# Kernel tuning notes

Measured on AMD Instinct MI355X. Metric: run time of the kernel, lower is better.

The kernel has to match this reference:

```python
import jax, jax.numpy as jnp
import numpy as np

N_NODES = 50000
N_EDGES = 800000
HID = 64


def fake_quant_w(w):
    # symmetric per-tensor int8 fake quantization (num_bits=8)
    s = jnp.maximum(jnp.max(jnp.abs(w)) / 127.0, 1e-8)
    q = jnp.clip(jnp.round(w / s), -127.0, 127.0) * s
    return w + jax.lax.stop_gradient(q - w)


def layer_norm(x, g, b, eps=1e-5):
    mu = jnp.mean(x, axis=-1, keepdims=True)
    var = jnp.var(x, axis=-1, keepdims=True)
    return (x - mu) * jax.lax.rsqrt(var + eps) * g + b


def pointnet_conv(x, pos, src, dst, W, n_nodes):
    # message: cat([x_j, pos_j - pos_i]) @ W_q^T, max-aggregated at i (dst)
    rel = pos[src] - pos[dst]                       # [E, 3]
    feat = jnp.concatenate([x[src], rel], axis=-1)  # [E, C+3]
    msg = feat @ fake_quant_w(W).T                  # [E, 64]
    h = jax.ops.segment_max(msg, dst, num_segments=n_nodes)
    return jnp.where(jnp.isfinite(h), h, 0.0)       # empty segments -> 0


def setup_inputs() -> dict:
    key = jax.random.key(0)
    ks = jax.random.split(key, 16)
    d = {}
    d["x"] = jax.random.normal(ks[0], (N_NODES, 1), jnp.float32)
    d["pos"] = jax.random.normal(ks[1], (N_NODES, 3), jnp.float32)
    d["edge_index"] = jax.random.randint(ks[2], (2, N_EDGES), 0, N_NODES, jnp.int32)
    sc = 0.02
    d["W0"] = jax.random.normal(ks[3], (HID, 1 + 3), jnp.float32) * sc
    d["Ws"] = jax.random.normal(ks[4], (4, HID, HID + 3), jnp.float32) * sc
    d["ln_g"] = jnp.ones((5, HID), jnp.float32)
    d["ln_b"] = jnp.zeros((5, HID), jnp.float32)
    d["mlp_w1"] = jax.random.normal(ks[5], (128, 320), jnp.float32) * sc
    d["mlp_b1"] = jnp.zeros((128,), jnp.float32)
    d["mlp_w2"] = jax.random.normal(ks[6], (128, 128), jnp.float32) * sc
    d["mlp_b2"] = jnp.zeros((128,), jnp.float32)
    d["mlp_w3"] = jax.random.normal(ks[7], (64, 128), jnp.float32) * sc
    d["mlp_b3"] = jnp.zeros((64,), jnp.float32)
    d["mlp_w4"] = jax.random.normal(ks[8], (2, 64), jnp.float32) * sc
    d["mlp_b4"] = jnp.zeros((2,), jnp.float32)
    d["scale"] = jnp.ones((2,), jnp.float32)
    return d


def reference(x, pos, edge_index, W0, Ws, ln_g, ln_b,
              mlp_w1, mlp_b1, mlp_w2, mlp_b2, mlp_w3, mlp_b3, mlp_w4, mlp_b4,
              scale):
    src, dst = edge_index[0], edge_index[1]
    n = x.shape[0]
    embeddings = []
    h = x
    for i in range(5):
        W = W0 if i == 0 else Ws[i - 1]
        h = pointnet_conv(h, pos, src, dst, W, n)
        h = layer_norm(h, ln_g[i], ln_b[i])
        h = jax.nn.relu(h)
        embeddings.append(h)
    z = jnp.concatenate(embeddings, axis=-1)  # [N, 320]
    z = layer_norm(z, jnp.ones((z.shape[-1],), z.dtype), jnp.zeros((z.shape[-1],), z.dtype))
    z = jax.nn.relu(z @ mlp_w1.T + mlp_b1)
    z = jax.nn.relu(z @ mlp_w2.T + mlp_b2)
    z = jax.nn.relu(z @ mlp_w3.T + mlp_b3)
    flow = (z @ mlp_w4.T + mlp_b4) * scale
    return flow
```

## Files before the change

kernel.cpp:

```cpp
#include <hip/hip_runtime.h>
#include <hip/hip_bf16.h>

#define N_NODES 50000
#define N_EDGES 800000
#define NBLK 196

__device__ __forceinline__ float bf2f(unsigned short u) {
    union { unsigned int i; float f; } c; c.i = ((unsigned int)u) << 16; return c.f;
}
__device__ __forceinline__ unsigned short f2bf(float f) {
    union { float f; unsigned int u; } c; c.f = f;
    unsigned int u = c.u;
    u += 0x7fffu + ((u >> 16) & 1u);
    return (unsigned short)(u >> 16);
}
__device__ __forceinline__ float ldin(const void* p, long i, int f32) {
    return f32 ? ((const float*)p)[i] : bf2f(((const unsigned short*)p)[i]);
}
__device__ __forceinline__ float wsum(float v) {
#pragma unroll
    for (int m = 32; m; m >>= 1) v += __shfl_xor(v, m, 64);
    return v;
}

__global__ void probe_kernel(const unsigned short* __restrict__ lng, int* __restrict__ flag) {
    if (threadIdx.x == 0 && blockIdx.x == 0)
        flag[0] = (lng[0] == 0x3F80 && lng[1] == 0x3F80) ? 0 : 1;
}

__global__ __launch_bounds__(256) void hist_kernel(const int* __restrict__ ei, int* __restrict__ deg) {
    int e = blockIdx.x * 256 + threadIdx.x;
    if (e < N_EDGES) atomicAdd(&deg[ei[N_EDGES + e]], 1);
}

__global__ __launch_bounds__(256) void bsum_kernel(const int* __restrict__ deg,
                                                   int* __restrict__ bsum) {
    __shared__ int wt[4];
    const int t = threadIdx.x, lane = t & 63, wid = t >> 6;
    const int i = blockIdx.x * 256 + t;
    int v = (i < N_NODES) ? deg[i] : 0;
    int r = v;
#pragma unroll
    for (int m = 32; m; m >>= 1) r += __shfl_xor(r, m, 64);
    if (lane == 0) wt[wid] = r;
    __syncthreads();
    if (t == 0) bsum[blockIdx.x] = wt[0] + wt[1] + wt[2] + wt[3];
}

__global__ __launch_bounds__(256) void boff_kernel(const int* __restrict__ bsum,
                                                   int* __restrict__ boff) {
    __shared__ int wt[4];
    const int t = threadIdx.x, lane = t & 63, wid = t >> 6;
    int v = (t < NBLK) ? bsum[t] : 0;
    int inc = v;
#pragma unroll
    for (int off = 1; off < 64; off <<= 1) {
        int u = __shfl_up(inc, off, 64);
        if (lane >= off) inc += u;
    }
    if (lane == 63) wt[wid] = inc;
    __syncthreads();
    int woff = 0;
    for (int w = 0; w < wid; ++w) woff += wt[w];
    if (t < NBLK) boff[t] = inc - v + woff;
}

__global__ __launch_bounds__(256) void scanout_kernel(const int* __restrict__ deg,
                                                      const int* __restrict__ boff,
                                                      int* __restrict__ rowptr,
                                                      int* __restrict__ cursor) {
    __shared__ int wt[4];
    const int t = threadIdx.x, lane = t & 63, wid = t >> 6;
    const int i = blockIdx.x * 256 + t;
    int v = (i < N_NODES) ? deg[i] : 0;
    int inc = v;
#pragma unroll
    for (int off = 1; off < 64; off <<= 1) {
        int u = __shfl_up(inc, off, 64);
        if (lane >= off) inc += u;
    }
    if (lane == 63) wt[wid] = inc;
    __syncthreads();
    int woff = 0;
    for (int w = 0; w < wid; ++w) woff += wt[w];
    int excl = inc - v + woff + boff[blockIdx.x];
    if (i < N_NODES) {
        rowptr[i] = excl;
        cursor[i] = excl;
        if (i == N_NODES - 1) rowptr[N_NODES] = excl + v;
    }
}

__global__ __launch_bounds__(256) void scatter_kernel(const int* __restrict__ ei,
                                                      int* __restrict__ cursor,
                                                      int* __restrict__ csr_src) {
    int e = blockIdx.x * 256 + threadIdx.x;
    if (e < N_EDGES) {
        int src = ei[e];
        int dst = ei[N_EDGES + e];
        int p = atomicAdd(&cursor[dst], 1);
        csr_src[p] = src;
    }
}

__global__ __launch_bounds__(256) void quant_kernel(const void* __restrict__ W0,
                                                    const void* __restrict__ Ws,
                                                    float* __restrict__ Wc0,
                                                    float* __restrict__ Wc,
                                                    const int* __restrict__ flagp) {
    const int f32 = *flagp;
    int layer = blockIdx.x;
    const void* src = (layer == 0) ? W0 : Ws;
    long sbase = (layer == 0) ? 0 : (long)(layer - 1) * 4288;
    float* dstc = (layer == 0) ? Wc0 : Wc + (size_t)(layer - 1) * 4352;
    int Ki = (layer == 0) ? 4 : 67;
    int n = 64 * Ki;
    __shared__ float red[256];
    float amax = 0.0f;
    for (int i = threadIdx.x; i < n; i += 256) amax = fmaxf(amax, fabsf(ldin(src, sbase + i, f32)));
    red[threadIdx.x] = amax;
    __syncthreads();
    for (int s = 128; s > 0; s >>= 1) {
        if (threadIdx.x < s) red[threadIdx.x] = fmaxf(red[threadIdx.x], red[threadIdx.x + s]);
        __syncthreads();
    }
    float sc = fmaxf(red[0] / 127.0f, 1e-8f);
    for (int i = threadIdx.x; i < n; i += 256) {
        float w = ldin(src, sbase + i, f32);
        float q = rintf(w / sc);
        q = fminf(fmaxf(q, -127.0f), 127.0f);
        int o = i / Ki, k = i % Ki;
        dstc[(size_t)k * 64 + o] = q * sc;
    }
}

__global__ __launch_bounds__(256) void u0_kernel(const void* __restrict__ x,
                                                 const void* __restrict__ pos,
                                                 const float* __restrict__ Wc0,
                                                 float* __restrict__ u,
                                                 const int* __restrict__ flagp) {
    const int f32 = *flagp;
    const int n = blockIdx.x * 256 + threadIdx.x;
    if (n >= N_NODES) return;
    const float xv = ldin(x, n, f32);
    const float p0 = ldin(pos, 3L * n + 0, f32);
    const float p1 = ldin(pos, 3L * n + 1, f32);
    const float p2 = ldin(pos, 3L * n + 2, f32);
    float4* up = reinterpret_cast<float4*>(u + (size_t)n * 64);
#pragma unroll
    for (int q = 0; q < 16; ++q) {
        const float4 w0 = *reinterpret_cast<const float4*>(Wc0 + 0 * 64 + 4 * q);
        const float4 w1 = *reinterpret_cast<const float4*>(Wc0 + 1 * 64 + 4 * q);
        const float4 w2 = *reinterpret_cast<const float4*>(Wc0 + 2 * 64 + 4 * q);
        const float4 w3 = *reinterpret_cast<const float4*>(Wc0 + 3 * 64 + 4 * q);
        float4 o;
        o.x = fmaf(p2, w3.x, fmaf(p1, w2.x, fmaf(p0, w1.x, xv * w0.x)));
        o.y = fmaf(p2, w3.y, fmaf(p1, w2.y, fmaf(p0, w1.y, xv * w0.y)));
        o.z = fmaf(p2, w3.z, fmaf(p1, w2.z, fmaf(p0, w1.z, xv * w0.z)));
        o.w = fmaf(p2, w3.w, fmaf(p1, w2.w, fmaf(p0, w1.w, xv * w0.w)));
        up[q] = o;
    }
}

__global__ __launch_bounds__(256) void agg_kernel(const float* __restrict__ u,
                                                  const void* __restrict__ pos,
                                                  const int* __restrict__ rowptr,
                                                  const int* __restrict__ csr,
                                                  const float* __restrict__ WcV, int vrow,
                                                  const float* __restrict__ WcN,
                                                  float* __restrict__ unext,
                                                  const void* __restrict__ lng,
                                                  const void* __restrict__ lnb,
                                                  int lnoff,
                                                  float* __restrict__ z, int out_off,
                                                  const int* __restrict__ flagp) {
    const int f32 = *flagp;
    const int lane = threadIdx.x & 63;
    const int n = (blockIdx.x * 256 + threadIdx.x) >> 6;
    if (n >= N_NODES) return;
    const int e0 = rowptr[n], e1 = rowptr[n + 1];
    float acc = -INFINITY;
    int e = e0;
    for (; e + 4 <= e1; e += 4) {
        const int s0 = csr[e + 0];
        const int s1 = csr[e + 1];
        const int s2 = csr[e + 2];
        const int s3 = csr[e + 3];
        const float a = u[(size_t)s0 * 64 + lane];
        const float b = u[(size_t)s1 * 64 + lane];
        const float c = u[(size_t)s2 * 64 + lane];
        const float d = u[(size_t)s3 * 64 + lane];
        acc = fmaxf(acc, fmaxf(fmaxf(a, b), fmaxf(c, d)));
    }
    for (; e < e1; ++e)
        acc = fmaxf(acc, u[(size_t)csr[e] * 64 + lane]);
    const float p0 = ldin(pos, 3L * n + 0, f32);
    const float p1 = ldin(pos, 3L * n + 1, f32);
    const float p2 = ldin(pos, 3L * n + 2, f32);
    const float v = fmaf(p2, WcV[(size_t)(vrow + 2) * 64 + lane],
                    fmaf(p1, WcV[(size_t)(vrow + 1) * 64 + lane],
                         p0 * WcV[(size_t)(vrow + 0) * 64 + lane]));
    float h = acc - v;
    if (!isfinite(h)) h = 0.0f;
    const float g = ldin(lng, lnoff + lane, f32);
    const float bb = ldin(lnb, lnoff + lane, f32);
    const float mu = wsum(h) * (1.0f / 64.0f);
    const float dd = h - mu;
    const float var = wsum(dd * dd) * (1.0f / 64.0f);
    float y = dd * rsqrtf(var + 1e-5f) * g + bb;
    y = fmaxf(y, 0.0f);
    z[(size_t)n * 320 + out_off + lane] = y;
    if (WcN) {
        float un = fmaf(p2, WcN[66 * 64 + lane],
                   fmaf(p1, WcN[65 * 64 + lane],
                        p0 * WcN[64 * 64 + lane]));
#pragma unroll
        for (int k = 0; k < 64; ++k)
            un = fmaf(__shfl(y, k, 64), WcN[k * 64 + lane], un);
        unext[(size_t)n * 64 + lane] = un;
    }
}

__global__ __launch_bounds__(256) void lnz_kernel(float* __restrict__ z) {
    const int lane = threadIdx.x & 63;
    const int gw = (blockIdx.x * blockDim.x + threadIdx.x) >> 6;
    const int nw = (gridDim.x * blockDim.x) >> 6;
    for (int nidx = gw; nidx < N_NODES; nidx += nw) {
        float v[5];
        float s = 0.f;
#pragma unroll
        for (int j = 0; j < 5; ++j) {
            v[j] = z[(size_t)nidx * 320 + j * 64 + lane];
            s += v[j];
        }
        float mu = wsum(s) * (1.0f / 320.0f);
        float q = 0.f;
#pragma unroll
        for (int j = 0; j < 5; ++j) { float d = v[j] - mu; q = fmaf(d, d, q); }
        float var = wsum(q) * (1.0f / 320.0f);
        float rs = rsqrtf(var + 1e-5f);
#pragma unroll
        for (int j = 0; j < 5; ++j) z[(size_t)nidx * 320 + j * 64 + lane] = (v[j] - mu) * rs;
    }
}

__global__ __launch_bounds__(256) void gemm_kernel(const float* __restrict__ A,
                                                   const void* __restrict__ W,
                                                   const void* __restrict__ bias,
                                                   float* __restrict__ C,
                                                   int Ki, int Ko,
                                                   const int* __restrict__ flagp) {
    __shared__ float At[16][68];
    __shared__ float Wt[16][68];
    const int f32 = *flagp;
    const int tid = threadIdx.x;
    const int bn = blockIdx.x * 64;
    const int bo = blockIdx.y * 64;
    const int o_base = (tid & 15) * 4;
    const int n_base = (tid >> 4) * 4;
    const int sr = tid >> 2;
    const int kq = (tid & 3) * 4;
    float acc[4][4] = {};
    for (int kk = 0; kk < Ki; kk += 16) {
        float4 av = make_float4(0.f, 0.f, 0.f, 0.f);
        if (bn + sr < N_NODES)
            av = *reinterpret_cast<const float4*>(A + (size_t)(bn + sr) * Ki + kk + kq);
        long wbase = (long)(bo + sr) * Ki + kk + kq;
        float wv0 = ldin(W, wbase + 0, f32);
        float wv1 = ldin(W, wbase + 1, f32);
        float wv2 = ldin(W, wbase + 2, f32);
        float wv3 = ldin(W, wbase + 3, f32);
        __syncthreads();
        At[kq + 0][sr] = av.x; At[kq + 1][sr] = av.y; At[kq + 2][sr] = av.z; At[kq + 3][sr] = av.w;
        Wt[kq + 0][sr] = wv0;  Wt[kq + 1][sr] = wv1;  Wt[kq + 2][sr] = wv2;  Wt[kq + 3][sr] = wv3;
        __syncthreads();
#pragma unroll
        for (int k = 0; k < 16; ++k) {
            const float4 a4 = *reinterpret_cast<const float4*>(&At[k][n_base]);
            const float4 w4 = *reinterpret_cast<const float4*>(&Wt[k][o_base]);
            const float a[4] = { a4.x, a4.y, a4.z, a4.w };
            const float ww[4] = { w4.x, w4.y, w4.z, w4.w };
#pragma unroll
            for (int i = 0; i < 4; ++i)
#pragma unroll
                for (int j = 0; j < 4; ++j)
                    acc[i][j] = fmaf(a[i], ww[j], acc[i][j]);
        }
    }
    float bj[4];
#pragma unroll
    for (int j = 0; j < 4; ++j) bj[j] = ldin(bias, bo + o_base + j, f32);
#pragma unroll
    for (int i = 0; i < 4; ++i) {
        int n = bn + n_base + i;
        if (n < N_NODES) {
#pragma unroll
            for (int j = 0; j < 4; ++j) {
                float c = fmaxf(acc[i][j] + bj[j], 0.0f);
                C[(size_t)n * Ko + bo + o_base + j] = c;
            }
        }
    }
}

__global__ __launch_bounds__(256) void out_kernel(const float* __restrict__ h3,
                                                  const void* __restrict__ w4,
                                                  const void* __restrict__ b4,
                                                  const void* __restrict__ scale,
                                                  void* __restrict__ out,
                                                  const int* __restrict__ flagp) {
    const int f32 = *flagp;
    const int lane = threadIdx.x & 63;
    const int gw = (blockIdx.x * blockDim.x + threadIdx.x) >> 6;
    const int nw = (gridDim.x * blockDim.x) >> 6;
    const float wa = ldin(w4, lane, f32);
    const float wb = ldin(w4, 64 + lane, f32);
    const float b0 = ldin(b4, 0, f32), b1 = ldin(b4, 1, f32);
    const float s0 = ldin(scale, 0, f32), s1 = ldin(scale, 1, f32);
    for (int nidx = gw; nidx < N_NODES; nidx += nw) {
        float h = h3[(size_t)nidx * 64 + lane];
        float d0 = wsum(h * wa);
        float d1 = wsum(h * wb);
        if (lane == 0) {
            float o0 = (d0 + b0) * s0;
            float o1 = (d1 + b1) * s1;
            if (f32) {
                ((float*)out)[nidx * 2 + 0] = o0;
                ((float*)out)[nidx * 2 + 1] = o1;
            } else {
                ((unsigned short*)out)[nidx * 2 + 0] = f2bf(o0);
                ((unsigned short*)out)[nidx * 2 + 1] = f2bf(o1);
            }
        }
    }
}

extern "C" void kernel_launch(void* const* d_in, const int* in_sizes, int n_in,
                              void* d_out, int out_size, void* d_ws, size_t ws_size,
                              hipStream_t stream) {
    (void)in_sizes; (void)n_in; (void)out_size; (void)ws_size;
    const void* x    = d_in[0];
    const void* pos  = d_in[1];
    const int*  ei   = (const int*)d_in[2];
    const void* W0   = d_in[3];
    const void* Ws   = d_in[4];
    const void* lng  = d_in[5];
    const void* lnb  = d_in[6];
    const void* w1   = d_in[7];
    const void* b1   = d_in[8];
    const void* w2   = d_in[9];
    const void* b2   = d_in[10];
    const void* w3   = d_in[11];
    const void* b3   = d_in[12];
    const void* w4   = d_in[13];
    const void* b4   = d_in[14];
    const void* scl  = d_in[15];

    float* z      = (float*)d_ws;
    float* h1     = z + 16000000;
    float* Wc0    = h1 + 6400000;
    float* Wc     = Wc0 + 256;
    int*   deg    = (int*)(Wc + 17408);
    int*   rowptr = deg + N_NODES;
    int*   cursor = rowptr + (N_NODES + 1);
    int*   flag   = cursor + N_NODES;
    int*   csr    = flag + 1;
    int*   bsum   = csr + N_EDGES;
    int*   boff   = bsum + 256;
    float* ua     = h1;
    float* ub     = h1 + 3200000;
    float* h2 = z;
    float* h3 = z + 6400000;

    hipMemsetAsync(deg, 0, N_NODES * sizeof(int), stream);
    probe_kernel<<<1, 64, 0, stream>>>((const unsigned short*)lng, flag);
    hist_kernel<<<(N_EDGES + 255) / 256, 256, 0, stream>>>(ei, deg);
    bsum_kernel<<<NBLK, 256, 0, stream>>>(deg, bsum);
    boff_kernel<<<1, 256, 0, stream>>>(bsum, boff);
    scanout_kernel<<<NBLK, 256, 0, stream>>>(deg, boff, rowptr, cursor);
    scatter_kernel<<<(N_EDGES + 255) / 256, 256, 0, stream>>>(ei, cursor, csr);
    quant_kernel<<<5, 256, 0, stream>>>(W0, Ws, Wc0, Wc, flag);

    const int gagg = (N_NODES * 64 + 255) / 256;

    u0_kernel<<<NBLK, 256, 0, stream>>>(x, pos, Wc0, ua, flag);
    agg_kernel<<<gagg, 256, 0, stream>>>(ua, pos, rowptr, csr,
                                         Wc0, 1, Wc + 0 * 4352, ub,
                                         lng, lnb, 0, z, 0, flag);
    agg_kernel<<<gagg, 256, 0, stream>>>(ub, pos, rowptr, csr,
                                         Wc + 0 * 4352, 64, Wc + 1 * 4352, ua,
                                         lng, lnb, 64, z, 64, flag);
    agg_kernel<<<gagg, 256, 0, stream>>>(ua, pos, rowptr, csr,
                                         Wc + 1 * 4352, 64, Wc + 2 * 4352, ub,
                                         lng, lnb, 128, z, 128, flag);
    agg_kernel<<<gagg, 256, 0, stream>>>(ub, pos, rowptr, csr,
                                         Wc + 2 * 4352, 64, Wc + 3 * 4352, ua,
                                         lng, lnb, 192, z, 192, flag);
    agg_kernel<<<gagg, 256, 0, stream>>>(ua, pos, rowptr, csr,
                                         Wc + 3 * 4352, 64, nullptr, nullptr,
                                         lng, lnb, 256, z, 256, flag);

    lnz_kernel<<<512, 256, 0, stream>>>(z);

    dim3 g1((N_NODES + 63) / 64, 2);
    gemm_kernel<<<g1, 256, 0, stream>>>(z, w1, b1, h1, 320, 128, flag);
    dim3 g2((N_NODES + 63) / 64, 2);
    gemm_kernel<<<g2, 256, 0, stream>>>(h1, w2, b2, h2, 128, 128, flag);
    dim3 g3((N_NODES + 63) / 64, 1);
    gemm_kernel<<<g3, 256, 0, stream>>>(h2, w3, b3, h3, 128, 64, flag);
    out_kernel<<<512, 256, 0, stream>>>(h3, w4, b4, scl, d_out, flag);
}
```

Before: 616.4 us.

## Split per-node layer transform into tiled GEMM kernel and prefetch GEMM tiles

Moves the next-layer linear transform out of the wave-per-node aggregation kernel, where it used 64 shuffles per node, into a separate LDS-tiled register-blocked GEMM kernel that reads the layer output from z, using a row-major copy of the quantized weights. It also pre-converts the MLP weights to fp32 so the GEMM kernel can use float4 loads, software-prefetches the next k-tile in the GEMM, and unrolls the gather-max loop to 8 with a scalarised node index. The cost is four extra kernel launches and an extra round trip of z and u through memory for each layer.

```diff
diff --git a/kernel.cpp b/kernel.cpp
--- a/kernel.cpp
+++ b/kernel.cpp
@@ -107,12 +107,14 @@
                                                     const void* __restrict__ Ws,
                                                     float* __restrict__ Wc0,
                                                     float* __restrict__ Wc,
+                                                    float* __restrict__ Wr,
                                                     const int* __restrict__ flagp) {
     const int f32 = *flagp;
     int layer = blockIdx.x;
     const void* src = (layer == 0) ? W0 : Ws;
     long sbase = (layer == 0) ? 0 : (long)(layer - 1) * 4288;
     float* dstc = (layer == 0) ? Wc0 : Wc + (size_t)(layer - 1) * 4352;
+    float* dstr = (layer == 0) ? nullptr : Wr + (size_t)(layer - 1) * 4352;
     int Ki = (layer == 0) ? 4 : 67;
     int n = 64 * Ki;
     __shared__ float red[256];
@@ -129,9 +131,23 @@
         float w = ldin(src, sbase + i, f32);
         float q = rintf(w / sc);
         q = fminf(fmaxf(q, -127.0f), 127.0f);
+        float v = q * sc;
         int o = i / Ki, k = i % Ki;
-        dstc[(size_t)k * 64 + o] = q * sc;
-    }
+        dstc[(size_t)k * 64 + o] = v;
+        if (dstr) dstr[(size_t)o * 68 + k] = v;
+    }
+}
+
+__global__ __launch_bounds__(256) void wcvt_kernel(const void* __restrict__ w1,
+                                                   const void* __restrict__ w2,
+                                                   const void* __restrict__ w3,
+                                                   float* __restrict__ Wm,
+                                                   const int* __restrict__ flagp) {
+    const int f32 = *flagp;
+    const int i = blockIdx.x * 256 + threadIdx.x;
+    if (i < 40960) Wm[i] = ldin(w1, i, f32);
+    else if (i < 57344) Wm[i] = ldin(w2, i - 40960, f32);
+    else if (i < 65536) Wm[i] = ldin(w3, i - 57344, f32);
 }
 
 __global__ __launch_bounds__(256) void u0_kernel(const void* __restrict__ x,
@@ -167,8 +183,6 @@
                                                   const int* __restrict__ rowptr,
                                                   const int* __restrict__ csr,
                                                   const float* __restrict__ WcV, int vrow,
-                                                  const float* __restrict__ WcN,
-                                                  float* __restrict__ unext,
                                                   const void* __restrict__ lng,
                                                   const void* __restrict__ lnb,
                                                   int lnoff,
@@ -176,21 +190,23 @@
                                                   const int* __restrict__ flagp) {
     const int f32 = *flagp;
     const int lane = threadIdx.x & 63;
-    const int n = (blockIdx.x * 256 + threadIdx.x) >> 6;
+    const int n = __builtin_amdgcn_readfirstlane((blockIdx.x * 256 + threadIdx.x) >> 6);
     if (n >= N_NODES) return;
     const int e0 = rowptr[n], e1 = rowptr[n + 1];
     float acc = -INFINITY;
     int e = e0;
-    for (; e + 4 <= e1; e += 4) {
-        const int s0 = csr[e + 0];
-        const int s1 = csr[e + 1];
-        const int s2 = csr[e + 2];
-        const int s3 = csr[e + 3];
-        const float a = u[(size_t)s0 * 64 + lane];
-        const float b = u[(size_t)s1 * 64 + lane];
-        const float c = u[(size_t)s2 * 64 + lane];
-        const float d = u[(size_t)s3 * 64 + lane];
-        acc = fmaxf(acc, fmaxf(fmaxf(a, b), fmaxf(c, d)));
+    for (; e + 8 <= e1; e += 8) {
+        const float a0 = u[(size_t)csr[e + 0] * 64 + lane];
+        const float a1 = u[(size_t)csr[e + 1] * 64 + lane];
+        const float a2 = u[(size_t)csr[e + 2] * 64 + lane];
+        const float a3 = u[(size_t)csr[e + 3] * 64 + lane];
+        const float a4 = u[(size_t)csr[e + 4] * 64 + lane];
+        const float a5 = u[(size_t)csr[e + 5] * 64 + lane];
+        const float a6 = u[(size_t)csr[e + 6] * 64 + lane];
+        const float a7 = u[(size_t)csr[e + 7] * 64 + lane];
+        const float m0 = fmaxf(fmaxf(a0, a1), fmaxf(a2, a3));
+        const float m1 = fmaxf(fmaxf(a4, a5), fmaxf(a6, a7));
+        acc = fmaxf(acc, fmaxf(m0, m1));
     }
     for (; e < e1; ++e)
         acc = fmaxf(acc, u[(size_t)csr[e] * 64 + lane]);
@@ -210,14 +226,69 @@
     float y = dd * rsqrtf(var + 1e-5f) * g + bb;
     y = fmaxf(y, 0.0f);
     z[(size_t)n * 320 + out_off + lane] = y;
-    if (WcN) {
-        float un = fmaf(p2, WcN[66 * 64 + lane],
-                   fmaf(p1, WcN[65 * 64 + lane],
-                        p0 * WcN[64 * 64 + lane]));
-#pragma unroll
-        for (int k = 0; k < 64; ++k)
-            un = fmaf(__shfl(y, k, 64), WcN[k * 64 + lane], un);
-        unext[(size_t)n * 64 + lane] = un;
+}
+
+__global__ __launch_bounds__(256) void un_kernel(const float* __restrict__ z, int in_off,
+                                                 const float* __restrict__ Wr,
+                                                 const void* __restrict__ pos,
+                                                 float* __restrict__ un,
+                                                 const int* __restrict__ flagp) {
+    __shared__ float At[16][68];
+    __shared__ float Wt[16][68];
+    const int f32 = *flagp;
+    const int tid = threadIdx.x;
+    const int bn = blockIdx.x * 64;
+    const int o_base = (tid & 15) * 4;
+    const int n_base = (tid >> 4) * 4;
+    const int sr = tid >> 2;
+    const int kq = (tid & 3) * 4;
+    float acc[4][4] = {};
+    float4 av = make_float4(0.f, 0.f, 0.f, 0.f);
+    if (bn + sr < N_NODES)
+        av = *reinterpret_cast<const float4*>(z + (size_t)(bn + sr) * 320 + in_off + kq);
+    float4 wv = *reinterpret_cast<const float4*>(Wr + (size_t)sr * 68 + kq);
+    for (int kk = 0; kk < 64; kk += 16) {
+        __syncthreads();
+        At[kq + 0][sr] = av.x; At[kq + 1][sr] = av.y; At[kq + 2][sr] = av.z; At[kq + 3][sr] = av.w;
+        Wt[kq + 0][sr] = wv.x; Wt[kq + 1][sr] = wv.y; Wt[kq + 2][sr] = wv.z; Wt[kq + 3][sr] = wv.w;
+        __syncthreads();
+        if (kk + 16 < 64) {
+            av = make_float4(0.f, 0.f, 0.f, 0.f);
+            if (bn + sr < N_NODES)
+                av = *reinterpret_cast<const float4*>(z + (size_t)(bn + sr) * 320 + in_off + kk + 16 + kq);
+            wv = *reinterpret_cast<const float4*>(Wr + (size_t)sr * 68 + kk + 16 + kq);
+        }
+#pragma unroll
+        for (int k = 0; k < 16; ++k) {
+            const float4 a4 = *reinterpret_cast<const float4*>(&At[k][n_base]);
+            const float4 w4 = *reinterpret_cast<const float4*>(&Wt[k][o_base]);
+            const float a[4] = { a4.x, a4.y, a4.z, a4.w };
+            const float ww[4] = { w4.x, w4.y, w4.z, w4.w };
+#pragma unroll
+            for (int i = 0; i < 4; ++i)
+#pragma unroll
+                for (int j = 0; j < 4; ++j)
+                    acc[i][j] = fmaf(a[i], ww[j], acc[i][j]);
+        }
+    }
+    float wp[3][4];
+#pragma unroll
+    for (int c = 0; c < 3; ++c)
+#pragma unroll
+        for (int j = 0; j < 4; ++j)
+            wp[c][j] = Wr[(size_t)(o_base + j) * 68 + 64 + c];
+#pragma unroll
+    for (int i = 0; i < 4; ++i) {
+        const int n = bn + n_base + i;
+        if (n < N_NODES) {
+            const float p0 = ldin(pos, 3L * n + 0, f32);
+            const float p1 = ldin(pos, 3L * n + 1, f32);
+            const float p2 = ldin(pos, 3L * n + 2, f32);
+#pragma unroll
+            for (int j = 0; j < 4; ++j)
+                un[(size_t)n * 64 + o_base + j] =
+                    fmaf(p2, wp[2][j], fmaf(p1, wp[1][j], fmaf(p0, wp[0][j], acc[i][j])));
+        }
     }
 }
 
@@ -245,7 +316,7 @@
 }
 
 __global__ __launch_bounds__(256) void gemm_kernel(const float* __restrict__ A,
-                                                   const void* __restrict__ W,
+                                                   const float* __restrict__ W,
                                                    const void* __restrict__ bias,
                                                    float* __restrict__ C,
                                                    int Ki, int Ko,
@@ -261,19 +332,21 @@
     const int sr = tid >> 2;
     const int kq = (tid & 3) * 4;
     float acc[4][4] = {};
+    float4 av = make_float4(0.f, 0.f, 0.f, 0.f);
+    if (bn + sr < N_NODES)
+        av = *reinterpret_cast<const float4*>(A + (size_t)(bn + sr) * Ki + kq);
+    float4 wv = *reinterpret_cast<const float4*>(W + (size_t)(bo + sr) * Ki + kq);
     for (int kk = 0; kk < Ki; kk += 16) {
-        float4 av = make_float4(0.f, 0.f, 0.f, 0.f);
-        if (bn + sr < N_NODES)
-            av = *reinterpret_cast<const float4*>(A + (size_t)(bn + sr) * Ki + kk + kq);
-        long wbase = (long)(bo + sr) * Ki + kk + kq;
-        float wv0 = ldin(W, wbase + 0, f32);
-        float wv1 = ldin(W, wbase + 1, f32);
-        float wv2 = ldin(W, wbase + 2, f32);
-        float wv3 = ldin(W, wbase + 3, f32);
         __syncthreads();
         At[kq + 0][sr] = av.x; At[kq + 1][sr] = av.y; At[kq + 2][sr] = av.z; At[kq + 3][sr] = av.w;
-        Wt[kq + 0][sr] = wv0;  Wt[kq + 1][sr] = wv1;  Wt[kq + 2][sr] = wv2;  Wt[kq + 3][sr] = wv3;
+        Wt[kq + 0][sr] = wv.x; Wt[kq + 1][sr] = wv.y; Wt[kq + 2][sr] = wv.z; Wt[kq + 3][sr] = wv.w;
         __syncthreads();
+        if (kk + 16 < Ki) {
+            av = make_float4(0.f, 0.f, 0.f, 0.f);
+            if (bn + sr < N_NODES)
+                av = *reinterpret_cast<const float4*>(A + (size_t)(bn + sr) * Ki + kk + 16 + kq);
+            wv = *reinterpret_cast<const float4*>(W + (size_t)(bo + sr) * Ki + kk + 16 + kq);
+        }
 #pragma unroll
         for (int k = 0; k < 16; ++k) {
             const float4 a4 = *reinterpret_cast<const float4*>(&At[k][n_base]);
@@ -360,13 +433,16 @@
     float* h1     = z + 16000000;
     float* Wc0    = h1 + 6400000;
     float* Wc     = Wc0 + 256;
-    int*   deg    = (int*)(Wc + 17408);
+    float* Wr     = Wc + 17408;
+    float* Wm     = Wr + 17408;
+    int*   deg    = (int*)(Wm + 65536);
     int*   rowptr = deg + N_NODES;
     int*   cursor = rowptr + (N_NODES + 1);
     int*   flag   = cursor + N_NODES;
     int*   csr    = flag + 1;
     int*   bsum   = csr + N_EDGES;
     int*   boff   = bsum + 256;
+    float* Wm1 = Wm, *Wm2 = Wm + 40960, *Wm3 = Wm + 57344;
     float* ua     = h1;
     float* ub     = h1 + 3200000;
     float* h2 = z;
@@ -379,34 +455,35 @@
     boff_kernel<<<1, 256, 0, stream>>>(bsum, boff);
     scanout_kernel<<<NBLK, 256, 0, stream>>>(deg, boff, rowptr, cursor);
     scatter_kernel<<<(N_EDGES + 255) / 256, 256, 0, stream>>>(ei, cursor, csr);
-    quant_kernel<<<5, 256, 0, stream>>>(W0, Ws, Wc0, Wc, flag);
+    quant_kernel<<<5, 256, 0, stream>>>(W0, Ws, Wc0, Wc, Wr, flag);
+    wcvt_kernel<<<256, 256, 0, stream>>>(w1, w2, w3, Wm, flag);
 
     const int gagg = (N_NODES * 64 + 255) / 256;
+    const int gun  = (N_NODES + 63) / 64;
 
     u0_kernel<<<NBLK, 256, 0, stream>>>(x, pos, Wc0, ua, flag);
-    agg_kernel<<<gagg, 256, 0, stream>>>(ua, pos, rowptr, csr,
-                                         Wc0, 1, Wc + 0 * 4352, ub,
+    agg_kernel<<<gagg, 256, 0, stream>>>(ua, pos, rowptr, csr, Wc0, 1,
                                          lng, lnb, 0, z, 0, flag);
-    agg_kernel<<<gagg, 256, 0, stream>>>(ub, pos, rowptr, csr,
-                                         Wc + 0 * 4352, 64, Wc + 1 * 4352, ua,
+    un_kernel<<<gun, 256, 0, stream>>>(z, 0, Wr + 0 * 4352, pos, ub, flag);
+    agg_kernel<<<gagg, 256, 0, stream>>>(ub, pos, rowptr, csr, Wc + 0 * 4352, 64,
                                          lng, lnb, 64, z, 64, flag);
-    agg_kernel<<<gagg, 256, 0, stream>>>(ua, pos, rowptr, csr,
-                                         Wc + 1 * 4352, 64, Wc + 2 * 4352, ub,
+    un_kernel<<<gun, 256, 0, stream>>>(z, 64, Wr + 1 * 4352, pos, ua, flag);
+    agg_kernel<<<gagg, 256, 0, stream>>>(ua, pos, rowptr, csr, Wc + 1 * 4352, 64,
                                          lng, lnb, 128, z, 128, flag);
-    agg_kernel<<<gagg, 256, 0, stream>>>(ub, pos, rowptr, csr,
-                                         Wc + 2 * 4352, 64, Wc + 3 * 4352, ua,
+    un_kernel<<<gun, 256, 0, stream>>>(z, 128, Wr + 2 * 4352, pos, ub, flag);
+    agg_kernel<<<gagg, 256, 0, stream>>>(ub, pos, rowptr, csr, Wc + 2 * 4352, 64,
                                          lng, lnb, 192, z, 192, flag);
-    agg_kernel<<<gagg, 256, 0, stream>>>(ua, pos, rowptr, csr,
-                                         Wc + 3 * 4352, 64, nullptr, nullptr,
+    un_kernel<<<gun, 256, 0, stream>>>(z, 192, Wr + 3 * 4352, pos, ua, flag);
+    agg_kernel<<<gagg, 256, 0, stream>>>(ua, pos, rowptr, csr, Wc + 3 * 4352, 64,
                                          lng, lnb, 256, z, 256, flag);
 
     lnz_kernel<<<512, 256, 0, stream>>>(z);
 
     dim3 g1((N_NODES + 63) / 64, 2);
-    gemm_kernel<<<g1, 256, 0, stream>>>(z, w1, b1, h1, 320, 128, flag);
+    gemm_kernel<<<g1, 256, 0, stream>>>(z, Wm1, b1, h1, 320, 128, flag);
     dim3 g2((N_NODES + 63) / 64, 2);
-    gemm_kernel<<<g2, 256, 0, stream>>>(h1, w2, b2, h2, 128, 128, flag);
+    gemm_kernel<<<g2, 256, 0, stream>>>(h1, Wm2, b2, h2, 128, 128, flag);
     dim3 g3((N_NODES + 63) / 64, 1);
-    gemm_kernel<<<g3, 256, 0, stream>>>(h2, w3, b3, h3, 128, 64, flag);
+    gemm_kernel<<<g3, 256, 0, stream>>>(h2, Wm3, b3, h3, 128, 64, flag);
     out_kernel<<<512, 256, 0, stream>>>(h3, w4, b4, scl, d_out, flag);
 }
```

Result: faster. 586.0 us (-4.9%).
